# Kernel tuning notes

Hardware: AMD Instinct MI355X
Metric: run time of the kernel (lower is better)

The kernel has to match this reference:

```python
import jax, jax.numpy as jnp
import numpy as np

EPROJS = 1024
DUNITS = 1024
AHEADS = 4
DK = 512
DV = 512
ACONV_CHANS = 128
ACONV_FILTS = 100
B = 16
T = 2048


def setup_inputs() -> dict:
    key = jax.random.key(0)
    ks = jax.random.split(key, 16)
    s = 0.02
    inp = {}
    inp["enc_hs_pad"] = jax.random.normal(ks[0], (B, T, EPROJS), jnp.float32)
    # lengths in [T//2, T] so no batch element is fully padded
    inp["enc_hs_len"] = jnp.sort(jax.random.randint(ks[1], (B,), T // 2, T + 1))
    inp["dec_z"] = jax.random.normal(ks[2], (B, DUNITS), jnp.float32)
    # per-head parameters, stacked on leading head axis where shapes match
    inp["Wq"] = jax.random.normal(ks[3], (AHEADS, DK, DUNITS), jnp.float32) * s
    inp["bq"] = jnp.zeros((AHEADS, DK), jnp.float32)
    inp["Wk"] = jax.random.normal(ks[4], (AHEADS, DK, EPROJS), jnp.float32) * s
    inp["Wv"] = jax.random.normal(ks[5], (AHEADS, DV, EPROJS), jnp.float32) * s
    inp["g_w"] = jax.random.normal(ks[6], (AHEADS, DK), jnp.float32) * s
    inp["g_b"] = jnp.zeros((AHEADS,), jnp.float32)
    inp["Watt"] = jax.random.normal(ks[7], (AHEADS, DK, ACONV_CHANS), jnp.float32) * s
    # conv kernels have DIFFERENT widths per head: 2*afilts+1, afilts = ACONV_FILTS*(h+1)//AHEADS
    for h in range(AHEADS):
        af = ACONV_FILTS * (h + 1) // AHEADS
        inp[f"conv_w_{h}"] = jax.random.normal(ks[8 + h], (ACONV_CHANS, 1, 2 * af + 1), jnp.float32) * s
    inp["Wo"] = jax.random.normal(ks[12], (EPROJS, AHEADS * DV), jnp.float32) * s
    return inp


def reference(enc_hs_pad, enc_hs_len, dec_z, Wq, bq, Wk, Wv, g_w, g_b, Watt,
              conv_w_0, conv_w_1, conv_w_2, conv_w_3, Wo):
    conv_ws = [conv_w_0, conv_w_1, conv_w_2, conv_w_3]
    Bb, Tt, _ = enc_hs_pad.shape
    scaling = jnp.float32(1.0) / jnp.sqrt(jnp.float32(DK))
    pos = jnp.arange(Tt)[None, :]                                   # (1,T)
    pad_mask = pos >= enc_hs_len[:, None]                           # (B,T) True at padding
    # att_prev=None path: uniform attention over valid frames (same for all heads)
    att_prev = (~pad_mask).astype(jnp.float32) / enc_hs_len[:, None].astype(jnp.float32)

    K = jnp.einsum('bte,hke->hbtk', enc_hs_pad, Wk)                 # pre_compute_k
    V = jnp.einsum('bte,hve->hbtv', enc_hs_pad, Wv)                 # pre_compute_v
    Q = jnp.einsum('bd,hkd->hbk', dec_z, Wq) + bq[:, None, :]       # mlp_q per head

    x = att_prev[:, None, :]                                        # (B,1,T) NCH
    cs, ws = [], []
    for h in range(AHEADS):  # heads have distinct conv widths -> structural loop
        wk = conv_ws[h]                                             # (C,1,2*af+1)
        af = (wk.shape[-1] - 1) // 2
        conv = jax.lax.conv_general_dilated(
            x, wk, window_strides=(1,), padding=[(af, af)],
            dimension_numbers=('NCH', 'OIH', 'NCH'))                # (B,C,T)
        att_feat = jnp.einsum('bct,kc->btk', conv, Watt[h])         # mlp_att
        e = jnp.einsum('btk,k->bt', jnp.tanh(K[h] + att_feat + Q[h][:, None, :]), g_w[h]) + g_b[h]
        e = jnp.where(pad_mask, -jnp.inf, e)
        w = jax.nn.softmax(scaling * e, axis=1)                     # (B,T)
        ws.append(w)
        cs.append(jnp.einsum('btv,bt->bv', V[h], w))                # weighted sum
    c = jnp.concatenate(cs, axis=1) @ Wo.T                          # (B,eprojs)
    return c, jnp.stack(ws)                                         # (B,eprojs), (H,B,T)
```

## Files before the change

### kernel.cpp

```cpp
#include <hip/hip_runtime.h>

#define EPROJS 1024
#define DUNITS 1024
#define AHEADS 4
#define DK 512
#define DV 512
#define CCH 128
#define BB 16
#define TT 2048

typedef __attribute__((ext_vector_type(8))) short bf16x8;
typedef __attribute__((ext_vector_type(4))) float f32x4;

static __device__ __forceinline__ short f2bf(float x) {
  unsigned u = __float_as_uint(x);
  unsigned r = u + 0x7fffu + ((u >> 16) & 1u);
  return (short)(r >> 16);
}
static __device__ __forceinline__ float bf2f(short x) {
  return __uint_as_float(((unsigned)(unsigned short)x) << 16);
}

static __device__ __forceinline__ float fast_tanh(float x) {
  float e2 = __expf(2.0f * x);
  return 1.0f - 2.0f / (e2 + 1.0f);
}

__global__ __launch_bounds__(256) void cvt_kernel(const float* __restrict__ in,
                                                  short* __restrict__ out, int n4) {
  int i = blockIdx.x * blockDim.x + threadIdx.x;
  if (i >= n4) return;
  float4 v = reinterpret_cast<const float4*>(in)[i];
  short4 o;
  o.x = f2bf(v.x); o.y = f2bf(v.y); o.z = f2bf(v.z); o.w = f2bf(v.w);
  reinterpret_cast<short4*>(out)[i] = o;
}

__global__ __launch_bounds__(256) void packB_kernel(const float* __restrict__ Wk,
                                                    const float* __restrict__ Watt,
                                                    short* __restrict__ Bp) {
  int idx = blockIdx.x * 256 + threadIdx.x;
  if (idx >= 294912) return;
  int lane = idx & 63; int t = idx >> 6;
  int nblk = t & 31; t >>= 5;
  int kkidx = t % 36; int h = t / 36;
  int col = nblk * 16 + (lane & 15);
  int k0 = kkidx * 32 + (lane >> 4) * 8;
  const float* src;
  if (k0 < 1024) src = Wk + ((size_t)(h * DK + col)) * EPROJS + k0;
  else           src = Watt + ((size_t)(h * DK + col)) * CCH + (k0 - 1024);
  float4 v0 = reinterpret_cast<const float4*>(src)[0];
  float4 v1 = reinterpret_cast<const float4*>(src)[1];
  short o[8] = { f2bf(v0.x), f2bf(v0.y), f2bf(v0.z), f2bf(v0.w),
                 f2bf(v1.x), f2bf(v1.y), f2bf(v1.z), f2bf(v1.w) };
  *reinterpret_cast<bf16x8*>(Bp + (size_t)idx * 8) = *reinterpret_cast<bf16x8*>(o);
}

__global__ __launch_bounds__(128) void prefix_kernel(const float* __restrict__ w0,
                                                     const float* __restrict__ w1,
                                                     const float* __restrict__ w2,
                                                     const float* __restrict__ w3,
                                                     float* __restrict__ S) {
  int h = blockIdx.x, c = threadIdx.x;
  const float* wk = (h == 0) ? w0 : (h == 1) ? w1 : (h == 2) ? w2 : w3;
  int af = (100 * (h + 1)) >> 2;
  int L = 2 * af + 1;
  float* Sh = S + h * 202 * 128;
  float s = 0.f;
  Sh[c] = 0.f;
  for (int t = 0; t < L; ++t) { s += wk[c * L + t]; Sh[(t + 1) * 128 + c] = s; }
}

__global__ __launch_bounds__(256) void q_kernel(const float* __restrict__ dec,
                                                const float* __restrict__ Wq,
                                                const float* __restrict__ bq,
                                                float* __restrict__ Qb) {
  int wid = (blockIdx.x * blockDim.x + threadIdx.x) >> 6;
  int lane = threadIdx.x & 63;
  int k = wid & (DK - 1); int hb = wid >> 9; int b = hb & (BB - 1); int h = hb >> 4;
  const float4* d4 = reinterpret_cast<const float4*>(dec + b * DUNITS);
  const float4* w4 = reinterpret_cast<const float4*>(Wq + (size_t)(h * DK + k) * DUNITS);
  float s = 0.f;
#pragma unroll
  for (int j = 0; j < 4; ++j) {
    float4 a = d4[j * 64 + lane], w = w4[j * 64 + lane];
    s += a.x * w.x + a.y * w.y + a.z * w.z + a.w * w.w;
  }
#pragma unroll
  for (int off = 32; off; off >>= 1) s += __shfl_xor(s, off);
  if (lane == 0) Qb[wid] = s + bq[h * DK + k];
}

__global__ __launch_bounds__(512, 3) void e_kernel(const short* __restrict__ encb,
                                                   const short* __restrict__ Bp,
                                                   const float* __restrict__ S,
                                                   const float* __restrict__ Qb,
                                                   const float* __restrict__ gw,
                                                   const int* __restrict__ lens,
                                                   float* __restrict__ ebuf) {
  __shared__ short At[2][64 * 128];
  __shared__ float epart[8][64];

  int bid = blockIdx.x;
  int xcd = bid & 7; int q = bid >> 3;
  int h = q & 3; int gq = q >> 2;
  int g = xcd + (gq << 3);
  int b = g >> 5; int t0 = (g & 31) << 6;

  int tid = threadIdx.x; int w = tid >> 6; int l = tid & 63;
  int lrow = l & 15, lhi = l >> 4;
  int len = lens[b];
  float invlen = 1.0f / (float)len;
  int af = (100 * (h + 1)) >> 2;

  const short* encB = encb + ((size_t)(b * TT + t0)) * EPROJS;
  const short* BpH = Bp + (size_t)h * 589824;

  int srow = tid >> 3;
  int sc = tid & 7;
  int wo0 = srow * 128 + ((sc ^ (srow & 7)) << 3);
  int wo1 = srow * 128 + (((sc + 8) ^ (srow & 7)) << 3);
  const short* sbase = encB + (size_t)srow * EPROJS + sc * 8;
  int rx = lrow & 7;

  bf16x8 bnext[4];
#pragma unroll
  for (int n = 0; n < 4; ++n)
    bnext[n] = *reinterpret_cast<const bf16x8*>(BpH + (w * 4 + n) * 512 + l * 8);

  bf16x8 s0 = *reinterpret_cast<const bf16x8*>(sbase);
  bf16x8 s1 = *reinterpret_cast<const bf16x8*>(sbase + 64);

  f32x4 acc[4][4] = {};

  *reinterpret_cast<bf16x8*>(&At[0][wo0]) = s0;
  *reinterpret_cast<bf16x8*>(&At[0][wo1]) = s1;

  const float* Sh = S + h * 202 * 128;

  for (int tl = 0; tl < 9; ++tl) {
    if (tl < 7) {
      s0 = *reinterpret_cast<const bf16x8*>(sbase + (tl + 1) * 128);
      s1 = *reinterpret_cast<const bf16x8*>(sbase + (tl + 1) * 128 + 64);
    } else if (tl == 7) {
      int t = t0 + srow;
      int lo = af - t; if (lo < 0) lo = 0;
      int hi = af - t + len - 1; if (hi > 2 * af) hi = 2 * af;
      bool any = (hi >= lo);
      const float* Plo = Sh + lo * 128;
      const float* Phi = Sh + (hi + 1) * 128;
      short o0[8], o1[8];
#pragma unroll
      for (int e = 0; e < 8; ++e) {
        int c = sc * 8 + e;
        float v0 = any ? (Phi[c] - Plo[c]) * invlen : 0.f;
        float v1 = any ? (Phi[c + 64] - Plo[c + 64]) * invlen : 0.f;
        o0[e] = f2bf(v0); o1[e] = f2bf(v1);
      }
      s0 = *reinterpret_cast<bf16x8*>(o0);
      s1 = *reinterpret_cast<bf16x8*>(o1);
    }
    __syncthreads();
#pragma unroll
    for (int kk = 0; kk < 4; ++kk) {
      bf16x8 bcur[4];
#pragma unroll
      for (int n = 0; n < 4; ++n) bcur[n] = bnext[n];
      int nk = tl * 4 + kk + 1;
      if (nk < 36) {
        const short* bp = BpH + (size_t)nk * 16384 + l * 8;
#pragma unroll
        for (int n = 0; n < 4; ++n)
          bnext[n] = *reinterpret_cast<const bf16x8*>(bp + (w * 4 + n) * 512);
      }
      bf16x8 afr[4];
      int x = ((kk * 4 + lhi) ^ rx) << 3;
#pragma unroll
      for (int m = 0; m < 4; ++m)
        afr[m] = *reinterpret_cast<const bf16x8*>(&At[tl & 1][(m * 16 + lrow) * 128 + x]);
#pragma unroll
      for (int m = 0; m < 4; ++m)
#pragma unroll
        for (int n = 0; n < 4; ++n)
          acc[m][n] = __builtin_amdgcn_mfma_f32_16x16x32_bf16(afr[m], bcur[n], acc[m][n], 0, 0, 0);
    }
    if (tl < 8) {
      int nb = (tl + 1) & 1;
      *reinterpret_cast<bf16x8*>(&At[nb][wo0]) = s0;
      *reinterpret_cast<bf16x8*>(&At[nb][wo1]) = s1;
    }
  }

  float part[4][4];
#pragma unroll
  for (int m = 0; m < 4; ++m)
#pragma unroll
    for (int r = 0; r < 4; ++r) part[m][r] = 0.f;

#pragma unroll
  for (int n = 0; n < 4; ++n) {
    int col = w * 64 + n * 16 + lrow;
    float qv = Qb[(h * BB + b) * DK + col];
    float gv = gw[h * DK + col];
#pragma unroll
    for (int m = 0; m < 4; ++m)
#pragma unroll
      for (int r = 0; r < 4; ++r)
        part[m][r] += fast_tanh(acc[m][n][r] + qv) * gv;
  }
#pragma unroll
  for (int off = 1; off < 16; off <<= 1)
#pragma unroll
    for (int m = 0; m < 4; ++m)
#pragma unroll
      for (int r = 0; r < 4; ++r) part[m][r] += __shfl_xor(part[m][r], off);

  if (lrow == 0) {
#pragma unroll
    for (int m = 0; m < 4; ++m)
#pragma unroll
      for (int r = 0; r < 4; ++r) epart[w][m * 16 + lhi * 4 + r] = part[m][r];
  }
  __syncthreads();
  if (tid < 64) {
    float s = 0.f;
#pragma unroll
    for (int ww = 0; ww < 8; ++ww) s += epart[ww][tid];
    ebuf[(size_t)(h * BB + b) * TT + t0 + tid] = s;
  }
}

__global__ __launch_bounds__(256) void softmax_kernel(const float* __restrict__ ebuf,
                                                      const int* __restrict__ lens,
                                                      float* __restrict__ wout) {
  int hb = blockIdx.x; int b = hb & (BB - 1);
  int tid = threadIdx.x;
  int len = lens[b];
  const float scaling = 0.04419417382415922f;
  const float* er = ebuf + (size_t)hb * TT;
  float vals[8];
  float mx = -1e30f;
#pragma unroll
  for (int j = 0; j < 8; ++j) {
    int t = j * 256 + tid;
    float v = (t < len) ? scaling * er[t] : -1e30f;
    vals[j] = v; mx = fmaxf(mx, v);
  }
  __shared__ float red[256];
  red[tid] = mx; __syncthreads();
  for (int s2 = 128; s2; s2 >>= 1) { if (tid < s2) red[tid] = fmaxf(red[tid], red[tid + s2]); __syncthreads(); }
  mx = red[0]; __syncthreads();
  float sum = 0.f;
#pragma unroll
  for (int j = 0; j < 8; ++j) {
    int t = j * 256 + tid;
    vals[j] = (t < len) ? __expf(vals[j] - mx) : 0.f;
    sum += vals[j];
  }
  red[tid] = sum; __syncthreads();
  for (int s2 = 128; s2; s2 >>= 1) { if (tid < s2) red[tid] += red[tid + s2]; __syncthreads(); }
  float inv = 1.f / red[0];
#pragma unroll
  for (int j = 0; j < 8; ++j)
    wout[(size_t)hb * TT + j * 256 + tid] = vals[j] * inv;
}

__global__ __launch_bounds__(256) void zero_kernel(float* __restrict__ p, int n) {
  int i = blockIdx.x * blockDim.x + threadIdx.x;
  if (i < n) p[i] = 0.f;
}

__global__ __launch_bounds__(256) void ctx_kernel(const short* __restrict__ encb,
                                                  const float* __restrict__ wout,
                                                  float* __restrict__ ctx) {
  int bid = blockIdx.x;
  int tc = bid & 7; int ec = (bid >> 3) & 3; int b = bid >> 5;
  int tid = threadIdx.x;
  int ecol = ec * 256 + tid;
  int t0 = tc * 256;
  __shared__ float wls[4][256];
#pragma unroll
  for (int h = 0; h < 4; ++h) wls[h][tid] = wout[(size_t)(h * BB + b) * TT + t0 + tid];
  __syncthreads();
  float a0 = 0.f, a1 = 0.f, a2 = 0.f, a3 = 0.f;
  const short* ep = encb + ((size_t)(b * TT + t0)) * EPROJS + ecol;
  for (int t2 = 0; t2 < 256; ++t2) {
    float v = bf2f(ep[(size_t)t2 * EPROJS]);
    a0 += wls[0][t2] * v; a1 += wls[1][t2] * v; a2 += wls[2][t2] * v; a3 += wls[3][t2] * v;
  }
  atomicAdd(&ctx[(0 * BB + b) * EPROJS + ecol], a0);
  atomicAdd(&ctx[(1 * BB + b) * EPROJS + ecol], a1);
  atomicAdd(&ctx[(2 * BB + b) * EPROJS + ecol], a2);
  atomicAdd(&ctx[(3 * BB + b) * EPROJS + ecol], a3);
}

__global__ __launch_bounds__(256) void cv_kernel(const float* __restrict__ ctx,
                                                 const float* __restrict__ Wv,
                                                 float* __restrict__ cvb) {
  int wid = (blockIdx.x * blockDim.x + threadIdx.x) >> 6;
  int lane = threadIdx.x & 63;
  int v = wid & (DV - 1); int h = wid >> 9;
  const float4* w4 = reinterpret_cast<const float4*>(Wv + (size_t)(h * DV + v) * EPROJS);
  float acc[BB];
#pragma unroll
  for (int b = 0; b < BB; ++b) acc[b] = 0.f;
#pragma unroll
  for (int j = 0; j < 4; ++j) {
    float4 ww = w4[j * 64 + lane];
#pragma unroll
    for (int b = 0; b < BB; ++b) {
      float4 a = reinterpret_cast<const float4*>(ctx + (size_t)(h * BB + b) * EPROJS)[j * 64 + lane];
      acc[b] += a.x * ww.x + a.y * ww.y + a.z * ww.z + a.w * ww.w;
    }
  }
#pragma unroll
  for (int off = 32; off; off >>= 1)
#pragma unroll
    for (int b = 0; b < BB; ++b) acc[b] += __shfl_xor(acc[b], off);
  if (lane == 0) {
#pragma unroll
    for (int b = 0; b < BB; ++b) cvb[b * 2048 + h * DV + v] = acc[b];
  }
}

__global__ __launch_bounds__(256) void out_kernel(const float* __restrict__ cvb,
                                                  const float* __restrict__ Wo,
                                                  float* __restrict__ outc) {
  int p = (blockIdx.x * blockDim.x + threadIdx.x) >> 6;
  int lane = threadIdx.x & 63;
  const float4* w4 = reinterpret_cast<const float4*>(Wo + (size_t)p * 2048);
  float acc[BB];
#pragma unroll
  for (int b = 0; b < BB; ++b) acc[b] = 0.f;
#pragma unroll
  for (int j = 0; j < 8; ++j) {
    float4 ww = w4[j * 64 + lane];
#pragma unroll
    for (int b = 0; b < BB; ++b) {
      float4 a = reinterpret_cast<const float4*>(cvb + (size_t)b * 2048)[j * 64 + lane];
      acc[b] += a.x * ww.x + a.y * ww.y + a.z * ww.z + a.w * ww.w;
    }
  }
#pragma unroll
  for (int off = 32; off; off >>= 1)
#pragma unroll
    for (int b = 0; b < BB; ++b) acc[b] += __shfl_xor(acc[b], off);
  if (lane == 0) {
#pragma unroll
    for (int b = 0; b < BB; ++b) outc[b * 1024 + p] = acc[b];
  }
}

extern "C" void kernel_launch(void* const* d_in, const int* in_sizes, int n_in,
                              void* d_out, int out_size, void* d_ws, size_t ws_size,
                              hipStream_t stream) {
  const float* enc  = (const float*)d_in[0];
  const int*   lens = (const int*)d_in[1];
  const float* dec  = (const float*)d_in[2];
  const float* Wq   = (const float*)d_in[3];
  const float* bq   = (const float*)d_in[4];
  const float* Wk   = (const float*)d_in[5];
  const float* Wv   = (const float*)d_in[6];
  const float* gw   = (const float*)d_in[7];
  const float* Watt = (const float*)d_in[9];
  const float* cw0  = (const float*)d_in[10];
  const float* cw1  = (const float*)d_in[11];
  const float* cw2  = (const float*)d_in[12];
  const float* cw3  = (const float*)d_in[13];
  const float* Wo   = (const float*)d_in[14];
  float* out = (float*)d_out;

  char* ws = (char*)d_ws;
  short* Bp    = (short*)(ws);
  float* S     = (float*)(ws + 4718592);
  float* Qb    = (float*)(ws + 5132288);
  float* ebuf  = (float*)(ws + 5263360);
  float* ctx   = (float*)(ws + 6311936);
  float* cvb   = (float*)(ws + 6574080);
  short* encb  = (short*)(ws + 6815744);

  float* wsout = out + 16384;

  cvt_kernel<<<32768, 256, 0, stream>>>(enc, encb, 8388608);
  packB_kernel<<<1152, 256, 0, stream>>>(Wk, Watt, Bp);
  prefix_kernel<<<4, 128, 0, stream>>>(cw0, cw1, cw2, cw3, S);
  q_kernel<<<8192, 256, 0, stream>>>(dec, Wq, bq, Qb);
  zero_kernel<<<256, 256, 0, stream>>>(ctx, 65536);
  e_kernel<<<2048, 512, 0, stream>>>(encb, Bp, S, Qb, gw, lens, ebuf);
  softmax_kernel<<<64, 256, 0, stream>>>(ebuf, lens, wsout);
  ctx_kernel<<<512, 256, 0, stream>>>(encb, wsout, ctx);
  cv_kernel<<<512, 256, 0, stream>>>(ctx, Wv, cvb);
  out_kernel<<<256, 256, 0, stream>>>(cvb, Wo, out);
}
```

Baseline: 364.0 us.

## Merge prep kernels, use direct-to-LDS triple-buffered loads in e_kernel, vectorize ctx

Folds the conversion, weight packing, prefix-sum, Q projection and zeroing kernels into one launch to cut launch overhead. The e_kernel now streams encoder tiles straight into LDS with global_load_lds into a three-stage ring, using explicit vmcnt waits and barriers, and raises the occupancy hint. Its block-to-XCD swizzle is replaced by a plain head-major mapping. ctx_kernel switches to 16-byte vector loads with 8 columns per thread over fewer blocks, which reduces strided scalar loads but lowers parallelism.

New measurement: 1.239 ms. 240% more time.

```diff
diff --git a/kernel.cpp b/kernel.cpp
--- a/kernel.cpp
+++ b/kernel.cpp
@@ -12,6 +12,11 @@
 typedef __attribute__((ext_vector_type(8))) short bf16x8;
 typedef __attribute__((ext_vector_type(4))) float f32x4;
 
+#define GLL16(gsrc, ldst)                                                        \
+  __builtin_amdgcn_global_load_lds(                                              \
+      (const __attribute__((address_space(1))) void*)(gsrc),                     \
+      (__attribute__((address_space(3))) void*)(ldst), 16, 0, 0)
+
 static __device__ __forceinline__ short f2bf(float x) {
   unsigned u = __float_as_uint(x);
   unsigned r = u + 0x7fffu + ((u >> 16) & 1u);
@@ -20,93 +25,85 @@
 static __device__ __forceinline__ float bf2f(short x) {
   return __uint_as_float(((unsigned)(unsigned short)x) << 16);
 }
-
 static __device__ __forceinline__ float fast_tanh(float x) {
   float e2 = __expf(2.0f * x);
   return 1.0f - 2.0f / (e2 + 1.0f);
 }
 
-__global__ __launch_bounds__(256) void cvt_kernel(const float* __restrict__ in,
-                                                  short* __restrict__ out, int n4) {
-  int i = blockIdx.x * blockDim.x + threadIdx.x;
-  if (i >= n4) return;
-  float4 v = reinterpret_cast<const float4*>(in)[i];
-  short4 o;
-  o.x = f2bf(v.x); o.y = f2bf(v.y); o.z = f2bf(v.z); o.w = f2bf(v.w);
-  reinterpret_cast<short4*>(out)[i] = o;
-}
-
-__global__ __launch_bounds__(256) void packB_kernel(const float* __restrict__ Wk,
-                                                    const float* __restrict__ Watt,
-                                                    short* __restrict__ Bp) {
-  int idx = blockIdx.x * 256 + threadIdx.x;
-  if (idx >= 294912) return;
-  int lane = idx & 63; int t = idx >> 6;
-  int nblk = t & 31; t >>= 5;
-  int kkidx = t % 36; int h = t / 36;
-  int col = nblk * 16 + (lane & 15);
-  int k0 = kkidx * 32 + (lane >> 4) * 8;
-  const float* src;
-  if (k0 < 1024) src = Wk + ((size_t)(h * DK + col)) * EPROJS + k0;
-  else           src = Watt + ((size_t)(h * DK + col)) * CCH + (k0 - 1024);
-  float4 v0 = reinterpret_cast<const float4*>(src)[0];
-  float4 v1 = reinterpret_cast<const float4*>(src)[1];
-  short o[8] = { f2bf(v0.x), f2bf(v0.y), f2bf(v0.z), f2bf(v0.w),
-                 f2bf(v1.x), f2bf(v1.y), f2bf(v1.z), f2bf(v1.w) };
-  *reinterpret_cast<bf16x8*>(Bp + (size_t)idx * 8) = *reinterpret_cast<bf16x8*>(o);
-}
-
-__global__ __launch_bounds__(128) void prefix_kernel(const float* __restrict__ w0,
-                                                     const float* __restrict__ w1,
-                                                     const float* __restrict__ w2,
-                                                     const float* __restrict__ w3,
-                                                     float* __restrict__ S) {
-  int h = blockIdx.x, c = threadIdx.x;
-  const float* wk = (h == 0) ? w0 : (h == 1) ? w1 : (h == 2) ? w2 : w3;
-  int af = (100 * (h + 1)) >> 2;
-  int L = 2 * af + 1;
-  float* Sh = S + h * 202 * 128;
-  float s = 0.f;
-  Sh[c] = 0.f;
-  for (int t = 0; t < L; ++t) { s += wk[c * L + t]; Sh[(t + 1) * 128 + c] = s; }
-}
-
-__global__ __launch_bounds__(256) void q_kernel(const float* __restrict__ dec,
-                                                const float* __restrict__ Wq,
-                                                const float* __restrict__ bq,
-                                                float* __restrict__ Qb) {
-  int wid = (blockIdx.x * blockDim.x + threadIdx.x) >> 6;
-  int lane = threadIdx.x & 63;
-  int k = wid & (DK - 1); int hb = wid >> 9; int b = hb & (BB - 1); int h = hb >> 4;
-  const float4* d4 = reinterpret_cast<const float4*>(dec + b * DUNITS);
-  const float4* w4 = reinterpret_cast<const float4*>(Wq + (size_t)(h * DK + k) * DUNITS);
-  float s = 0.f;
-#pragma unroll
-  for (int j = 0; j < 4; ++j) {
-    float4 a = d4[j * 64 + lane], w = w4[j * 64 + lane];
-    s += a.x * w.x + a.y * w.y + a.z * w.z + a.w * w.w;
-  }
-#pragma unroll
-  for (int off = 32; off; off >>= 1) s += __shfl_xor(s, off);
-  if (lane == 0) Qb[wid] = s + bq[h * DK + k];
-}
-
-__global__ __launch_bounds__(512, 3) void e_kernel(const short* __restrict__ encb,
+__global__ __launch_bounds__(256) void prep_kernel(
+    const float* __restrict__ enc, short* __restrict__ encb,
+    const float* __restrict__ Wk, const float* __restrict__ Watt, short* __restrict__ Bp,
+    const float* __restrict__ w0, const float* __restrict__ w1,
+    const float* __restrict__ w2, const float* __restrict__ w3, float* __restrict__ S,
+    const float* __restrict__ dec, const float* __restrict__ Wq,
+    const float* __restrict__ bq, float* __restrict__ Qb,
+    float* __restrict__ ctx) {
+  int bid = blockIdx.x, tid = threadIdx.x;
+  if (bid < 32768) {
+    int i = bid * 256 + tid;
+    float4 v = reinterpret_cast<const float4*>(enc)[i];
+    short4 o;
+    o.x = f2bf(v.x); o.y = f2bf(v.y); o.z = f2bf(v.z); o.w = f2bf(v.w);
+    reinterpret_cast<short4*>(encb)[i] = o;
+  } else if (bid < 33920) {
+    int idx = (bid - 32768) * 256 + tid;
+    int lane = idx & 63; int t = idx >> 6;
+    int nblk = t & 31; t >>= 5;
+    int kkidx = t % 36; int h = t / 36;
+    int col = nblk * 16 + (lane & 15);
+    int k0 = kkidx * 32 + (lane >> 4) * 8;
+    const float* src;
+    if (k0 < 1024) src = Wk + ((size_t)(h * DK + col)) * EPROJS + k0;
+    else           src = Watt + ((size_t)(h * DK + col)) * CCH + (k0 - 1024);
+    float4 v0 = reinterpret_cast<const float4*>(src)[0];
+    float4 v1 = reinterpret_cast<const float4*>(src)[1];
+    short o[8] = { f2bf(v0.x), f2bf(v0.y), f2bf(v0.z), f2bf(v0.w),
+                   f2bf(v1.x), f2bf(v1.y), f2bf(v1.z), f2bf(v1.w) };
+    *reinterpret_cast<bf16x8*>(Bp + (size_t)idx * 8) = *reinterpret_cast<bf16x8*>(o);
+  } else if (bid < 33924) {
+    if (tid < 128) {
+      int h = bid - 33920, c = tid;
+      const float* wk = (h == 0) ? w0 : (h == 1) ? w1 : (h == 2) ? w2 : w3;
+      int af = (100 * (h + 1)) >> 2;
+      int L = 2 * af + 1;
+      float* Sh = S + h * 202 * 128;
+      float s = 0.f;
+      Sh[c] = 0.f;
+      for (int t = 0; t < L; ++t) { s += wk[c * L + t]; Sh[(t + 1) * 128 + c] = s; }
+    }
+  } else if (bid < 42116) {
+    int wid = ((bid - 33924) * 256 + tid) >> 6;
+    int lane = tid & 63;
+    int k = wid & (DK - 1); int hb = wid >> 9; int b = hb & (BB - 1); int h = hb >> 4;
+    const float4* d4 = reinterpret_cast<const float4*>(dec + b * DUNITS);
+    const float4* w4 = reinterpret_cast<const float4*>(Wq + (size_t)(h * DK + k) * DUNITS);
+    float s = 0.f;
+#pragma unroll
+    for (int j = 0; j < 4; ++j) {
+      float4 a = d4[j * 64 + lane], w = w4[j * 64 + lane];
+      s += a.x * w.x + a.y * w.y + a.z * w.z + a.w * w.w;
+    }
+#pragma unroll
+    for (int off = 32; off; off >>= 1) s += __shfl_xor(s, off);
+    if (lane == 0) Qb[wid] = s + bq[h * DK + k];
+  } else {
+    int i = (bid - 42116) * 256 + tid;
+    if (i < 65536) ctx[i] = 0.f;
+  }
+}
+
+__global__ __launch_bounds__(512, 6) void e_kernel(const short* __restrict__ encb,
                                                    const short* __restrict__ Bp,
                                                    const float* __restrict__ S,
                                                    const float* __restrict__ Qb,
                                                    const float* __restrict__ gw,
                                                    const int* __restrict__ lens,
                                                    float* __restrict__ ebuf) {
-  __shared__ short At[2][64 * 128];
+  __shared__ short At[3][64 * 128];
   __shared__ float epart[8][64];
 
   int bid = blockIdx.x;
-  int xcd = bid & 7; int q = bid >> 3;
-  int h = q & 3; int gq = q >> 2;
-  int g = xcd + (gq << 3);
-  int b = g >> 5; int t0 = (g & 31) << 6;
-
+  int h = bid >> 9; int rem = bid & 511; int b = rem >> 5; int t0 = (rem & 31) << 6;
   int tid = threadIdx.x; int w = tid >> 6; int l = tid & 63;
   int lrow = l & 15, lhi = l >> 4;
   int len = lens[b];
@@ -116,11 +113,12 @@
   const short* encB = encb + ((size_t)(b * TT + t0)) * EPROJS;
   const short* BpH = Bp + (size_t)h * 589824;
 
-  int srow = tid >> 3;
-  int sc = tid & 7;
-  int wo0 = srow * 128 + ((sc ^ (srow & 7)) << 3);
-  int wo1 = srow * 128 + (((sc + 8) ^ (srow & 7)) << 3);
-  const short* sbase = encB + (size_t)srow * EPROJS + sc * 8;
+  int ci0 = tid, ci1 = 512 + tid;
+  int r0 = ci0 >> 4, p0 = ci0 & 15;
+  int r1 = ci1 >> 4, p1 = ci1 & 15;
+  const short* g0 = encB + (size_t)r0 * EPROJS + ((p0 ^ (r0 & 7)) << 3);
+  const short* g1 = encB + (size_t)r1 * EPROJS + ((p1 ^ (r1 & 7)) << 3);
+  int d0 = ci0 * 8, d1 = ci1 * 8;
   int rx = lrow & 7;
 
   bf16x8 bnext[4];
@@ -128,24 +126,26 @@
   for (int n = 0; n < 4; ++n)
     bnext[n] = *reinterpret_cast<const bf16x8*>(BpH + (w * 4 + n) * 512 + l * 8);
 
-  bf16x8 s0 = *reinterpret_cast<const bf16x8*>(sbase);
-  bf16x8 s1 = *reinterpret_cast<const bf16x8*>(sbase + 64);
+  short* A0 = &At[0][0]; short* A1 = &At[1][0]; short* A2 = &At[2][0];
+
+  GLL16(g0, A0 + d0); GLL16(g1, A0 + d1);
+  GLL16(g0 + 128, A1 + d0); GLL16(g1 + 128, A1 + d1);
 
   f32x4 acc[4][4] = {};
 
-  *reinterpret_cast<bf16x8*>(&At[0][wo0]) = s0;
-  *reinterpret_cast<bf16x8*>(&At[0][wo1]) = s1;
+  __builtin_amdgcn_sched_barrier(0);
+  asm volatile("s_waitcnt vmcnt(2)" ::: "memory");
+  __builtin_amdgcn_s_barrier();
+  __builtin_amdgcn_sched_barrier(0);
 
   const float* Sh = S + h * 202 * 128;
 
-  for (int tl = 0; tl < 9; ++tl) {
-    if (tl < 7) {
-      s0 = *reinterpret_cast<const bf16x8*>(sbase + (tl + 1) * 128);
-      s1 = *reinterpret_cast<const bf16x8*>(sbase + (tl + 1) * 128 + 64);
-    } else if (tl == 7) {
-      int t = t0 + srow;
-      int lo = af - t; if (lo < 0) lo = 0;
-      int hi = af - t + len - 1; if (hi > 2 * af) hi = 2 * af;
+  for (int t = 0; t < 9; ++t) {
+    if (t == 6) {
+      int srow = tid >> 3, sc = tid & 7;
+      int tt = t0 + srow;
+      int lo = af - tt; if (lo < 0) lo = 0;
+      int hi = af - tt + len - 1; if (hi > 2 * af) hi = 2 * af;
       bool any = (hi >= lo);
       const float* Plo = Sh + lo * 128;
       const float* Phi = Sh + (hi + 1) * 128;
@@ -157,16 +157,17 @@
         float v1 = any ? (Phi[c + 64] - Plo[c + 64]) * invlen : 0.f;
         o0[e] = f2bf(v0); o1[e] = f2bf(v1);
       }
-      s0 = *reinterpret_cast<bf16x8*>(o0);
-      s1 = *reinterpret_cast<bf16x8*>(o1);
-    }
-    __syncthreads();
+      *reinterpret_cast<bf16x8*>(&A2[srow * 128 + ((sc ^ (srow & 7)) << 3)]) =
+          *reinterpret_cast<bf16x8*>(o0);
+      *reinterpret_cast<bf16x8*>(&A2[srow * 128 + (((sc + 8) ^ (srow & 7)) << 3)]) =
+          *reinterpret_cast<bf16x8*>(o1);
+    }
 #pragma unroll
     for (int kk = 0; kk < 4; ++kk) {
       bf16x8 bcur[4];
 #pragma unroll
       for (int n = 0; n < 4; ++n) bcur[n] = bnext[n];
-      int nk = tl * 4 + kk + 1;
+      int nk = t * 4 + kk + 1;
       if (nk < 36) {
         const short* bp = BpH + (size_t)nk * 16384 + l * 8;
 #pragma unroll
@@ -177,18 +178,28 @@
       int x = ((kk * 4 + lhi) ^ rx) << 3;
 #pragma unroll
       for (int m = 0; m < 4; ++m)
-        afr[m] = *reinterpret_cast<const bf16x8*>(&At[tl & 1][(m * 16 + lrow) * 128 + x]);
+        afr[m] = *reinterpret_cast<const bf16x8*>(&A0[(m * 16 + lrow) * 128 + x]);
 #pragma unroll
       for (int m = 0; m < 4; ++m)
 #pragma unroll
         for (int n = 0; n < 4; ++n)
           acc[m][n] = __builtin_amdgcn_mfma_f32_16x16x32_bf16(afr[m], bcur[n], acc[m][n], 0, 0, 0);
     }
-    if (tl < 8) {
-      int nb = (tl + 1) & 1;
-      *reinterpret_cast<bf16x8*>(&At[nb][wo0]) = s0;
-      *reinterpret_cast<bf16x8*>(&At[nb][wo1]) = s1;
-    }
+    if (t < 6) {
+      __builtin_amdgcn_sched_barrier(0);
+      const short* gs0 = g0 + (t + 2) * 128;
+      const short* gs1 = g1 + (t + 2) * 128;
+      GLL16(gs0, A2 + d0); GLL16(gs1, A2 + d1);
+    }
+    __builtin_amdgcn_sched_barrier(0);
+    if (t < 6) {
+      asm volatile("s_waitcnt vmcnt(6) lgkmcnt(0)" ::: "memory");
+    } else {
+      asm volatile("s_waitcnt vmcnt(4) lgkmcnt(0)" ::: "memory");
+    }
+    __builtin_amdgcn_s_barrier();
+    __builtin_amdgcn_sched_barrier(0);
+    short* tmp = A0; A0 = A1; A1 = A2; A2 = tmp;
   }
 
   float part[4][4];
@@ -265,33 +276,37 @@
     wout[(size_t)hb * TT + j * 256 + tid] = vals[j] * inv;
 }
 
-__global__ __launch_bounds__(256) void zero_kernel(float* __restrict__ p, int n) {
-  int i = blockIdx.x * blockDim.x + threadIdx.x;
-  if (i < n) p[i] = 0.f;
-}
-
 __global__ __launch_bounds__(256) void ctx_kernel(const short* __restrict__ encb,
                                                   const float* __restrict__ wout,
                                                   float* __restrict__ ctx) {
   int bid = blockIdx.x;
-  int tc = bid & 7; int ec = (bid >> 3) & 3; int b = bid >> 5;
+  int tc = bid & 7; int b = bid >> 3;
+  int t0 = tc * 256;
   int tid = threadIdx.x;
-  int ecol = ec * 256 + tid;
-  int t0 = tc * 256;
+  int chunk = tid & 127;
+  int rofs = tid >> 7;
   __shared__ float wls[4][256];
 #pragma unroll
   for (int h = 0; h < 4; ++h) wls[h][tid] = wout[(size_t)(h * BB + b) * TT + t0 + tid];
   __syncthreads();
-  float a0 = 0.f, a1 = 0.f, a2 = 0.f, a3 = 0.f;
-  const short* ep = encb + ((size_t)(b * TT + t0)) * EPROJS + ecol;
-  for (int t2 = 0; t2 < 256; ++t2) {
-    float v = bf2f(ep[(size_t)t2 * EPROJS]);
-    a0 += wls[0][t2] * v; a1 += wls[1][t2] * v; a2 += wls[2][t2] * v; a3 += wls[3][t2] * v;
-  }
-  atomicAdd(&ctx[(0 * BB + b) * EPROJS + ecol], a0);
-  atomicAdd(&ctx[(1 * BB + b) * EPROJS + ecol], a1);
-  atomicAdd(&ctx[(2 * BB + b) * EPROJS + ecol], a2);
-  atomicAdd(&ctx[(3 * BB + b) * EPROJS + ecol], a3);
+  float a0[8] = {}, a1[8] = {}, a2[8] = {}, a3[8] = {};
+  for (int t2 = rofs; t2 < 256; t2 += 2) {
+    bf16x8 v = *reinterpret_cast<const bf16x8*>(
+        encb + ((size_t)(b * TT + t0 + t2)) * EPROJS + chunk * 8);
+    float w0 = wls[0][t2], w1 = wls[1][t2], w2 = wls[2][t2], w3 = wls[3][t2];
+#pragma unroll
+    for (int e = 0; e < 8; ++e) {
+      float f = bf2f(v[e]);
+      a0[e] += w0 * f; a1[e] += w1 * f; a2[e] += w2 * f; a3[e] += w3 * f;
+    }
+  }
+#pragma unroll
+  for (int e = 0; e < 8; ++e) {
+    atomicAdd(&ctx[(0 * BB + b) * EPROJS + chunk * 8 + e], a0[e]);
+    atomicAdd(&ctx[(1 * BB + b) * EPROJS + chunk * 8 + e], a1[e]);
+    atomicAdd(&ctx[(2 * BB + b) * EPROJS + chunk * 8 + e], a2[e]);
+    atomicAdd(&ctx[(3 * BB + b) * EPROJS + chunk * 8 + e], a3[e]);
+  }
 }
 
 __global__ __launch_bounds__(256) void cv_kernel(const float* __restrict__ ctx,
@@ -381,14 +396,12 @@
 
   float* wsout = out + 16384;
 
-  cvt_kernel<<<32768, 256, 0, stream>>>(enc, encb, 8388608);
-  packB_kernel<<<1152, 256, 0, stream>>>(Wk, Watt, Bp);
-  prefix_kernel<<<4, 128, 0, stream>>>(cw0, cw1, cw2, cw3, S);
-  q_kernel<<<8192, 256, 0, stream>>>(dec, Wq, bq, Qb);
-  zero_kernel<<<256, 256, 0, stream>>>(ctx, 65536);
+  prep_kernel<<<42372, 256, 0, stream>>>(enc, encb, Wk, Watt, Bp,
+                                         cw0, cw1, cw2, cw3, S,
+                                         dec, Wq, bq, Qb, ctx);
   e_kernel<<<2048, 512, 0, stream>>>(encb, Bp, S, Qb, gw, lens, ebuf);
   softmax_kernel<<<64, 256, 0, stream>>>(ebuf, lens, wsout);
-  ctx_kernel<<<512, 256, 0, stream>>>(encb, wsout, ctx);
+  ctx_kernel<<<128, 256, 0, stream>>>(encb, wsout, ctx);
   cv_kernel<<<512, 256, 0, stream>>>(ctx, Wv, cvb);
   out_kernel<<<256, 256, 0, stream>>>(cvb, Wo, out);
 }
```
